# Optimization experiments

Measured on AMD Instinct MI355X. Metric: run time of the kernel, lower is better.

## Reference

```python
import jax, jax.numpy as jnp
import numpy as np
import math

B, N, L, ED, H = 2, 32, 4, 64, 4   # graphs, nodes/graph, layers, embed_dim, heads
HD = ED // H
EPS = 1e-5


def _ln(x, g, b):
    m = x.mean(-1, keepdims=True)
    v = ((x - m) ** 2).mean(-1, keepdims=True)
    return (x - m) * jax.lax.rsqrt(v + EPS) * g + b


def _layer(x, W, b, lg, lb, fW, fb, fg, fbeta):
    # NOTE: in the torch source, ModuleList([Linear]*4) shares ONE linear for
    # q/k/v1/v2 and ONE LayerNorm for norms[0..2]; we reproduce that sharing.
    h = (x @ W.T + b).reshape(B, N, N, H, HD)
    q = _ln(h, lg, lb)                                    # q == k (shared LN)
    scores = jnp.einsum('bxahd,bayhd->bxayh', q, q) / math.sqrt(HD)
    att = jax.nn.softmax(scores, axis=2)                  # softmax over 'a'
    xu = jnp.einsum('bxahd,bayhd->bxayhd', h, h)          # v1 == v2 == h
    xu = _ln(xu, lg, lb)                                  # shared LN again
    xu = jnp.einsum('bxayh,bxayhd->bxyhd', att, xu).reshape(B, N, N, ED)
    y = jnp.concatenate([x, xu], axis=-1) @ fW.T + fb
    return _ln(y, fg, fbeta)


def _diag_offdiag_maxpool(x):
    # x: (B, ED, N, N)
    diag = jnp.diagonal(x, axis1=-2, axis2=-1)            # (B, ED, N)
    max_diag = diag.max(axis=2)                           # (B, ED)
    val = jnp.abs(max_diag.max() + (-x).max())
    eye = jnp.eye(N, dtype=x.dtype)
    max_offdiag = (x - val * eye).max(axis=(2, 3))        # (B, ED)
    return jnp.concatenate([max_diag, max_offdiag], axis=1)  # (B, 2*ED)


def setup_inputs() -> dict:
    key = jax.random.key(0)
    ks = jax.random.split(key, 12)
    E = 1024
    g = jax.random.randint(ks[0], (E,), 0, B)
    ls = jax.random.randint(ks[1], (E,), 0, N)
    ld = jax.random.randint(ks[2], (E,), 0, N)
    edge_index = jnp.stack([g * N + ls, g * N + ld]).astype(jnp.int64)
    batch = (jnp.arange(B * N) // N).astype(jnp.int64)
    std = 0.02
    return {
        'edge_index': edge_index,
        'batch': batch,
        'W0': jax.random.normal(ks[3], (ED, 1), jnp.float32) * std,
        'b0': jnp.zeros((ED,), jnp.float32),
        'Ws': jax.random.normal(ks[4], (L - 1, ED, ED), jnp.float32) * std,
        'bs': jnp.zeros((L - 1, ED), jnp.float32),
        'ln_g': jnp.ones((L, HD), jnp.float32),
        'ln_b': jnp.zeros((L, HD), jnp.float32),
        'fW0': jax.random.normal(ks[5], (ED, 1 + ED), jnp.float32) * std,
        'fb0': jnp.zeros((ED,), jnp.float32),
        'fWs': jax.random.normal(ks[6], (L - 1, ED, 2 * ED), jnp.float32) * std,
        'fbs': jnp.zeros((L - 1, ED), jnp.float32),
        'fln_g': jnp.ones((L, ED), jnp.float32),
        'fln_b': jnp.zeros((L, ED), jnp.float32),
        'opW': jax.random.normal(ks[7], (L, ED // 2, 2 * ED), jnp.float32) * std,
        'opb': jnp.zeros((L, ED // 2), jnp.float32),
    }


def reference(edge_index, batch, W0, b0, Ws, bs, ln_g, ln_b,
              fW0, fb0, fWs, fbs, fln_g, fln_b, opW, opb):
    # to_dense_adj with edge_attr = 1.0
    g = batch[edge_index[0]]
    ls = edge_index[0] - g * N
    ld = edge_index[1] - g * N
    adj = jnp.zeros((B, N, N), jnp.float32).at[g, ls, ld].add(1.0)
    idx = jnp.arange(N)
    adj = adj.at[:, idx, idx].set(2.0)
    x = adj[..., None]                                    # (B, N, N, 1)

    scores = jnp.zeros((B, ED // 2), jnp.float32)
    for i in range(L):
        W = W0 if i == 0 else Ws[i - 1]
        b = b0 if i == 0 else bs[i - 1]
        fW = fW0 if i == 0 else fWs[i - 1]
        fb = fb0 if i == 0 else fbs[i - 1]
        x = _layer(x, W, b, ln_g[i], ln_b[i], fW, fb, fln_g[i], fln_b[i])
        pooled = _diag_offdiag_maxpool(jnp.transpose(x, (0, 3, 1, 2)))
        scores = scores + pooled @ opW[i].T + opb[i]

    # BatchNorm1d(momentum=1.0, affine=False), training mode -> batch stats
    m = scores.mean(axis=0)
    v = scores.var(axis=0)
    return (scores - m) / jnp.sqrt(v + EPS)
```

## Files before the change

### kernel.cpp

```cpp
#include <hip/hip_runtime.h>
#include <math.h>

#define EPS 1e-5f

#define AG_LOAD(p)     __hip_atomic_load((p), __ATOMIC_RELAXED, __HIP_MEMORY_SCOPE_AGENT)

__device__ __forceinline__ unsigned fenc(float f) {
    unsigned u = __float_as_uint(f);
    return (u & 0x80000000u) ? ~u : (u | 0x80000000u);
}
__device__ __forceinline__ float fdec(unsigned u) {
    u = (u & 0x80000000u) ? (u & 0x7FFFFFFFu) : ~u;
    return __uint_as_float(u);
}

struct Params {
    const int* ei; const int* batch; int E;
    const float* W0; const float* b0; const float* Ws; const float* bs;
    const float* ln_g; const float* ln_b;
    const float* fW0; const float* fb0; const float* fWs; const float* fbs;
    const float* fln_g; const float* fln_b;
    const float* opW; const float* opb;
    float* hA; float* hAT;
    float* hB; float* hBT;
    float* xbuf;
    unsigned* PdgU; unsigned* PoffU; unsigned* PmnU;
    int* bar;
    float* out;
};


__device__ __forceinline__ void pool_atomic(Params& p, int layer, int b_blk, int e,
                                            float mn, float off, float dg) {
    int o = layer * 128 + b_blk * 64 + e;
    atomicMax(&p.PdgU[o],  fenc(dg));
    atomicMax(&p.PoffU[o], fenc(off));
    atomicMax(&p.PmnU[o],  fenc(-mn));
}

__launch_bounds__(256, 2)
__global__ void k0(Params p) {
    const int tid  = threadIdx.x;
    const int blk  = blockIdx.x;
    const int gtid = blk * 256 + tid;
    const int c    = tid & 63;
    const int d    = c & 15;
    const int rl   = tid >> 6;
    const int rx   = rl >> 1;
    const int ry   = rl & 1;
    const int b_blk = blk >> 8;
    const int x0    = ((blk >> 4) & 15) * 2;
    const int y0    = (blk & 15) * 2;
    const int a_l  = c & 31;
    const int h1   = c >> 5;

    __shared__ float xslab2[2 * 32];
    __shared__ float yslab2[32 * 2];
    __shared__ __align__(16) float cA[64], cC[64], cW[64], cB0[64], cG[64], cBl[64];
    __shared__ float hstat[3][4];
    __shared__ float A1_s[4 * 132];
    __shared__ float K0h_s[4][4];
    __shared__ __align__(16) float xrow[4][64];
    __shared__ __align__(16) float xu_s[4][64];
    __shared__ float Wf0[64];
    __shared__ __align__(16) float T65[64 * 68];
    __shared__ __align__(16) float ST[64 * 68];

    if (tid < 64)  xslab2[tid] = 0.0f;
    if (tid >= 64 && tid < 128) yslab2[tid - 64] = 0.0f;

    if (tid < 64) {
        float Wc = p.W0[c], bc = p.b0[c];
        float sW = Wc, sB = bc;
        #pragma unroll
        for (int m = 1; m < 16; m <<= 1) {
            sW += __shfl_xor(sW, m, 16);
            sB += __shfl_xor(sB, m, 16);
        }
        float Ac = Wc - sW * 0.0625f;
        float Bc = bc - sB * 0.0625f;
        float sAA = Ac * Ac, sAB = Ac * Bc, sBB = Bc * Bc;
        #pragma unroll
        for (int m = 1; m < 16; m <<= 1) {
            sAA += __shfl_xor(sAA, m, 16);
            sAB += __shfl_xor(sAB, m, 16);
            sBB += __shfl_xor(sBB, m, 16);
        }
        cA[c] = Ac; cC[c] = Bc; cW[c] = Wc; cB0[c] = bc;
        cG[c] = p.ln_g[d]; cBl[c] = p.ln_b[d];
        if (d == 0) {
            hstat[0][c >> 4] = sAA * 0.0625f;
            hstat[1][c >> 4] = sAB * 0.0625f;
            hstat[2][c >> 4] = sBB * 0.0625f;
        }
        Wf0[tid] = p.fW0[tid * 65];
    }
    #pragma unroll
    for (int s = 0; s < 4; ++s) {
        int i = tid + s * 256;
        int cc = i >> 4, u = i & 15;
        const float* src = p.fW0 + cc * 65 + 1 + 4 * u;
        float4 w = make_float4(src[0], src[1], src[2], src[3]);
        *(float4*)(T65 + cc * 68 + 4 * ((u + 2 * cc) & 15)) = w;
    }
    #pragma unroll
    for (int s = 0; s < 4; ++s) {
        int i = tid + s * 256;
        float4 w = ((const float4*)p.Ws)[i];
        int cc = i >> 4, u = i & 15;
        *(float4*)(ST + cc * 68 + 4 * ((u + 2 * cc) & 15)) = w;
    }
    __syncthreads();

    for (int e2 = tid; e2 < p.E; e2 += 256) {
        int e0 = p.ei[e2], e1 = p.ei[p.E + e2];
        int g  = p.batch[e0];
        if (g == b_blk) {
            int ls = e0 - g * 32, ld = e1 - g * 32;
            unsigned dx = (unsigned)(ls - x0);
            if (dx < 2u) atomicAdd(&xslab2[dx * 32 + ld], 1.0f);
            unsigned dy = (unsigned)(ld - y0);
            if (dy < 2u) atomicAdd(&yslab2[ls * 2 + dy], 1.0f);
        }
    }
    __syncthreads();
    if (tid < 2)  xslab2[tid * 32 + x0 + tid] = 2.0f;
    if (tid >= 2 && tid < 4) { int j = tid - 2; yslab2[(y0 + j) * 2 + j] = 2.0f; }
    __syncthreads();

    const float vx = xslab2[rx * 32 + a_l];
    const float vy = yslab2[a_l * 2 + ry];
    float s0, s1, is0, is1, w0m, w1m;
    #pragma unroll
    for (int hb = 0; hb < 2; ++hb) {
        const int hh = h1 + 2 * hb;
        float rsx = rsqrtf(fmaf(fmaf(hstat[0][hh], vx, 2.0f * hstat[1][hh]), vx, hstat[2][hh]) + EPS);
        float rsy = rsqrtf(fmaf(fmaf(hstat[0][hh], vy, 2.0f * hstat[1][hh]), vy, hstat[2][hh]) + EPS);
        float qq = 0.f, sp = 0.f, sq = 0.f;
        #pragma unroll
        for (int t = 0; t < 4; ++t) {
            int dd = hh * 16 + 4 * t;
            float4 av = *(const float4*)(cA + dd);
            float4 bv = *(const float4*)(cC + dd);
            float4 wv = *(const float4*)(cW + dd);
            float4 b0v = *(const float4*)(cB0 + dd);
            float4 gv = *(const float4*)(cG + dd);
            float4 blv = *(const float4*)(cBl + dd);
            float qx, qy, pp;
            qx = fmaf(av.x, vx, bv.x) * rsx * gv.x + blv.x;
            qy = fmaf(av.x, vy, bv.x) * rsy * gv.x + blv.x;
            qq = fmaf(qx, qy, qq);
            pp = fmaf(wv.x, vx, b0v.x) * fmaf(wv.x, vy, b0v.x); sp += pp; sq += pp * pp;
            qx = fmaf(av.y, vx, bv.y) * rsx * gv.y + blv.y;
            qy = fmaf(av.y, vy, bv.y) * rsy * gv.y + blv.y;
            qq = fmaf(qx, qy, qq);
            pp = fmaf(wv.y, vx, b0v.y) * fmaf(wv.y, vy, b0v.y); sp += pp; sq += pp * pp;
            qx = fmaf(av.z, vx, bv.z) * rsx * gv.z + blv.z;
            qy = fmaf(av.z, vy, bv.z) * rsy * gv.z + blv.z;
            qq = fmaf(qx, qy, qq);
            pp = fmaf(wv.z, vx, b0v.z) * fmaf(wv.z, vy, b0v.z); sp += pp; sq += pp * pp;
            qx = fmaf(av.w, vx, bv.w) * rsx * gv.w + blv.w;
            qy = fmaf(av.w, vy, bv.w) * rsy * gv.w + blv.w;
            qq = fmaf(qx, qy, qq);
            pp = fmaf(wv.w, vx, b0v.w) * fmaf(wv.w, vy, b0v.w); sp += pp; sq += pp * pp;
        }
        float ss = qq * 0.25f;
        float mu = sp * 0.0625f, var = fmaxf(sq * 0.0625f - mu * mu, 0.f);
        float is = rsqrtf(var + EPS);
        if (hb == 0) { s0 = ss; is0 = is; w0m = mu * is; }
        else         { s1 = ss; is1 = is; w1m = mu * is; }
    }

    float m0 = s0, m1 = s1;
    #pragma unroll
    for (int m = 1; m < 32; m <<= 1) {
        m0 = fmaxf(m0, __shfl_xor(m0, m));
        m1 = fmaxf(m1, __shfl_xor(m1, m));
    }
    float e0 = __expf(s0 - m0), e1 = __expf(s1 - m1);
    float l0 = e0, l1 = e1, k0a = e0 * w0m, k1a = e1 * w1m;
    #pragma unroll
    for (int m = 1; m < 32; m <<= 1) {
        l0 += __shfl_xor(l0, m);  l1 += __shfl_xor(l1, m);
        k0a += __shfl_xor(k0a, m); k1a += __shfl_xor(k1a, m);
    }
    A1_s[rl * 132 + h1 * 33 + a_l]       = e0 * is0 / l0;
    A1_s[rl * 132 + (h1 + 2) * 33 + a_l] = e1 * is1 / l1;
    if (a_l == 0) {
        K0h_s[rl][h1]     = k0a / l0;
        K0h_s[rl][h1 + 2] = k1a / l1;
    }

    {
        const int hc = c >> 4;
        const float Wc = cW[c], bc = cB0[c];
        float acc = 0.f;
        #pragma unroll
        for (int a = 0; a < 32; ++a) {
            float vx2 = xslab2[rx * 32 + a];
            float vy2 = yslab2[a * 2 + ry];
            float pv = fmaf(Wc, vx2, bc) * fmaf(Wc, vy2, bc);
            acc = fmaf(A1_s[rl * 132 + hc * 33 + a], pv, acc);
        }
        xu_s[rl][c] = (acc - K0h_s[rl][hc]) * cG[c] + cBl[c];
    }

    const float adjv = xslab2[rx * 32 + y0 + ry];
    float acc2 = fmaf(Wf0[c], adjv, p.fb0[c]);
    #pragma unroll
    for (int u = 0; u < 16; ++u) {
        float4 w = *(const float4*)(T65 + c * 68 + 4 * ((u + 2 * c) & 15));
        float4 xr = *(const float4*)(&xu_s[rl][4 * u]);
        acc2 = fmaf(w.x, xr.x, acc2); acc2 = fmaf(w.y, xr.y, acc2);
        acc2 = fmaf(w.z, xr.z, acc2); acc2 = fmaf(w.w, xr.w, acc2);
    }
    float t1 = acc2;
    #pragma unroll
    for (int m = 1; m < 64; m <<= 1) t1 += __shfl_xor(t1, m, 64);
    float mu = t1 * (1.0f / 64.0f);
    float dv2 = acc2 - mu;
    float t2 = dv2 * dv2;
    #pragma unroll
    for (int m = 1; m < 64; m <<= 1) t2 += __shfl_xor(t2, m, 64);
    float xnew = dv2 * rsqrtf(t2 * (1.0f / 64.0f) + EPS) * p.fln_g[c] + p.fln_b[c];
    xrow[rl][c]  = xnew;
    p.xbuf[gtid] = xnew;
    __syncthreads();

    if (tid < 64) {
        float mn = 1e30f, off = -1e30f, dg = -1e30f;
        #pragma unroll
        for (int r2 = 0; r2 < 4; ++r2) {
            float v = xrow[r2][tid];
            mn = fminf(mn, v);
            if (x0 + (r2 >> 1) == y0 + (r2 & 1)) dg = fmaxf(dg, v);
            else off = fmaxf(off, v);
        }
        pool_atomic(p, 0, b_blk, tid, mn, off, dg);
    }

    {
        float acc = p.bs[c];
        #pragma unroll
        for (int u = 0; u < 16; ++u) {
            float4 w = *(const float4*)(ST + c * 68 + 4 * ((u + 2 * c) & 15));
            float4 xr = *(const float4*)(&xrow[rl][4 * u]);
            acc = fmaf(w.x, xr.x, acc); acc = fmaf(w.y, xr.y, acc);
            acc = fmaf(w.z, xr.z, acc); acc = fmaf(w.w, xr.w, acc);
        }
        int x = x0 + rx, y = y0 + ry;
        p.hA[(b_blk * 1024 + x * 32 + y) * 64 + c] = acc;
        p.hAT[((b_blk * 32 + y) * 32 + x) * 64 + c] = acc;
    }
}

__launch_bounds__(256, 2)
__global__ void klayer(Params p, int layer, int is_last) {
    const int tid  = threadIdx.x;
    const int blk  = blockIdx.x;
    const int gtid = blk * 256 + tid;
    const int c    = tid & 63;
    const int d    = c & 15;
    const int rl   = tid >> 6;
    const int rx   = rl >> 1;
    const int ry   = rl & 1;
    const int b_blk = blk >> 8;
    const int x0    = ((blk >> 4) & 15) * 2;
    const int y0    = (blk & 15) * 2;
    const int a_l  = c & 31;
    const int h1   = c >> 5;

    const float* hin  = (layer == 2) ? p.hB  : p.hA;
    const float* hinT = (layer == 2) ? p.hBT : p.hAT;
    float* hout  = (layer == 1) ? p.hB  : p.hA;
    float* houtT = (layer == 1) ? p.hBT : p.hAT;

    __shared__ __align__(16) float hx2_s[2][2176];
    __shared__ __align__(16) float yT2_s[2][2176];
    __shared__ __align__(16) float FT[64 * 132];
    __shared__ float A1_s[4 * 132];
    __shared__ float K0h_s[4][4];
    __shared__ __align__(16) float xrow[4][64];
    __shared__ __align__(16) float xu_s[4][64];
    __shared__ __align__(16) float g16[16], b16[16];
    __shared__ float vals[4];
    __shared__ float scores_s[64];
    __shared__ int tailflag;
    float* sm_mn  = &hx2_s[0][0];
    float* sm_off = sm_mn + 512;
    float* sm_dg  = sm_mn + 1024;
    float* psum   = sm_mn + 1536;

    float xv = p.xbuf[gtid];
    {
        const float4* sx0 = (const float4*)(hin + (b_blk * 1024 + x0 * 32) * 64);
        const float4* sx1 = (const float4*)(hin + (b_blk * 1024 + (x0 + 1) * 32) * 64);
        const float4* sy0 = (const float4*)(hinT + (b_blk * 32 + y0) * 2048);
        const float4* sy1 = (const float4*)(hinT + (b_blk * 32 + y0 + 1) * 2048);
        #pragma unroll
        for (int s = 0; s < 2; ++s) {
            int ii = tid + s * 256;
            int a = ii >> 4, u = ii & 15, pr = (u + 2 * a) & 15;
            *(float4*)(&hx2_s[0][a * 68 + 4 * pr]) = sx0[ii];
            *(float4*)(&hx2_s[1][a * 68 + 4 * pr]) = sx1[ii];
            *(float4*)(&yT2_s[0][a * 68 + 4 * pr]) = sy0[ii];
            *(float4*)(&yT2_s[1][a * 68 + 4 * pr]) = sy1[ii];
        }
    }
    if (tid < 16) {
        g16[tid] = p.ln_g[layer * 16 + tid];
        b16[tid] = p.ln_b[layer * 16 + tid];
    }
    {
        const float4* fw = (const float4*)(p.fWs + (layer - 1) * 8192);
        #pragma unroll
        for (int s = 0; s < 8; ++s) {
            int i = tid + s * 256;
            float4 w = fw[i];
            int cc = i >> 5, u = i & 31;
            *(float4*)(FT + cc * 132 + 4 * ((u + 2 * cc) & 31)) = w;
        }
    }
    xrow[rl][c] = xv;
    __syncthreads();

    float s0, s1, is0, is1, w0m, w1m;
    #pragma unroll
    for (int hb = 0; hb < 2; ++hb) {
        const int hh = h1 + 2 * hb;
        float4 xh4[4], yh4[4];
        float sxp = 0.f, sxq = 0.f, syp = 0.f, syq = 0.f;
        #pragma unroll
        for (int t = 0; t < 4; ++t) {
            int ps = 4 * (((hh * 4 + t) + 2 * a_l) & 15);
            float4 v = *(const float4*)(&hx2_s[rx][a_l * 68 + ps]);
            float4 y = *(const float4*)(&yT2_s[ry][a_l * 68 + ps]);
            xh4[t] = v; yh4[t] = y;
            sxp += v.x + v.y + v.z + v.w;
            sxq += v.x*v.x + v.y*v.y + v.z*v.z + v.w*v.w;
            syp += y.x + y.y + y.z + y.w;
            syq += y.x*y.x + y.y*y.y + y.z*y.z + y.w*y.w;
        }
        float mxm = sxp * 0.0625f;
        float rsx = rsqrtf(fmaxf(sxq * 0.0625f - mxm * mxm, 0.f) + EPS);
        float mym = syp * 0.0625f;
        float rsy = rsqrtf(fmaxf(syq * 0.0625f - mym * mym, 0.f) + EPS);
        float qq = 0.f, sp = 0.f, sq = 0.f;
        #pragma unroll
        for (int t = 0; t < 4; ++t) {
            float4 g4 = *(const float4*)(g16 + 4 * t);
            float4 b4 = *(const float4*)(b16 + 4 * t);
            float4 xh = xh4[t], yh = yh4[t];
            float qx, qy, pp;
            qx = (xh.x - mxm) * rsx * g4.x + b4.x;
            qy = (yh.x - mym) * rsy * g4.x + b4.x;
            qq = fmaf(qx, qy, qq);  pp = xh.x * yh.x; sp += pp; sq += pp * pp;
            qx = (xh.y - mxm) * rsx * g4.y + b4.y;
            qy = (yh.y - mym) * rsy * g4.y + b4.y;
            qq = fmaf(qx, qy, qq);  pp = xh.y * yh.y; sp += pp; sq += pp * pp;
            qx = (xh.z - mxm) * rsx * g4.z + b4.z;
            qy = (yh.z - mym) * rsy * g4.z + b4.z;
            qq = fmaf(qx, qy, qq);  pp = xh.z * yh.z; sp += pp; sq += pp * pp;
            qx = (xh.w - mxm) * rsx * g4.w + b4.w;
            qy = (yh.w - mym) * rsy * g4.w + b4.w;
            qq = fmaf(qx, qy, qq);  pp = xh.w * yh.w; sp += pp; sq += pp * pp;
        }
        float ss = qq * 0.25f;
        float mu = sp * 0.0625f, var = fmaxf(sq * 0.0625f - mu * mu, 0.f);
        float is = rsqrtf(var + EPS);
        if (hb == 0) { s0 = ss; is0 = is; w0m = mu * is; }
        else         { s1 = ss; is1 = is; w1m = mu * is; }
    }

    float m0 = s0, m1 = s1;
    #pragma unroll
    for (int m = 1; m < 32; m <<= 1) {
        m0 = fmaxf(m0, __shfl_xor(m0, m));
        m1 = fmaxf(m1, __shfl_xor(m1, m));
    }
    float e0 = __expf(s0 - m0), e1 = __expf(s1 - m1);
    float l0 = e0, l1 = e1, k0a = e0 * w0m, k1a = e1 * w1m;
    #pragma unroll
    for (int m = 1; m < 32; m <<= 1) {
        l0 += __shfl_xor(l0, m);  l1 += __shfl_xor(l1, m);
        k0a += __shfl_xor(k0a, m); k1a += __shfl_xor(k1a, m);
    }
    A1_s[rl * 132 + h1 * 33 + a_l]       = e0 * is0 / l0;
    A1_s[rl * 132 + (h1 + 2) * 33 + a_l] = e1 * is1 / l1;
    if (a_l == 0) {
        K0h_s[rl][h1]     = k0a / l0;
        K0h_s[rl][h1 + 2] = k1a / l1;
    }

    {
        const int hc = c >> 4;
        const int ce = c & 3;
        float acc = 0.f;
        #pragma unroll
        for (int a = 0; a < 32; ++a) {
            int ps = 4 * (((c >> 2) + 2 * a) & 15) + ce;
            float hxv = hx2_s[rx][a * 68 + ps];
            float hyv = yT2_s[ry][a * 68 + ps];
            acc = fmaf(A1_s[rl * 132 + hc * 33 + a], hxv * hyv, acc);
        }
        xu_s[rl][c] = (acc - K0h_s[rl][hc]) * g16[d] + b16[d];
    }

    float acc2 = p.fbs[(layer - 1) * 64 + c];
    #pragma unroll
    for (int u = 0; u < 16; ++u) {
        float4 w = *(const float4*)(FT + c * 132 + 4 * ((u + 2 * c) & 31));
        float4 xr = *(const float4*)(&xrow[rl][4 * u]);
        acc2 = fmaf(w.x, xr.x, acc2); acc2 = fmaf(w.y, xr.y, acc2);
        acc2 = fmaf(w.z, xr.z, acc2); acc2 = fmaf(w.w, xr.w, acc2);
    }
    #pragma unroll
    for (int u = 16; u < 32; ++u) {
        float4 w = *(const float4*)(FT + c * 132 + 4 * ((u + 2 * c) & 31));
        float4 xr = *(const float4*)(&xu_s[rl][4 * (u - 16)]);
        acc2 = fmaf(w.x, xr.x, acc2); acc2 = fmaf(w.y, xr.y, acc2);
        acc2 = fmaf(w.z, xr.z, acc2); acc2 = fmaf(w.w, xr.w, acc2);
    }
    float t1 = acc2;
    #pragma unroll
    for (int m = 1; m < 64; m <<= 1) t1 += __shfl_xor(t1, m, 64);
    float mu = t1 * (1.0f / 64.0f);
    float dv2 = acc2 - mu;
    float t2 = dv2 * dv2;
    #pragma unroll
    for (int m = 1; m < 64; m <<= 1) t2 += __shfl_xor(t2, m, 64);
    float xnew = dv2 * rsqrtf(t2 * (1.0f / 64.0f) + EPS) *
                 p.fln_g[layer * 64 + c] + p.fln_b[layer * 64 + c];
    __syncthreads();
    xrow[rl][c] = xnew;
    if (!is_last) {
        p.xbuf[gtid] = xnew;
        const float4* sw = (const float4*)(p.Ws + layer * 4096);
        #pragma unroll
        for (int s = 0; s < 4; ++s) {
            int i = tid + s * 256;
            float4 w = sw[i];
            int cc = i >> 4, u = i & 15;
            *(float4*)(FT + cc * 68 + 4 * ((u + 2 * cc) & 15)) = w;
        }
    }
    __syncthreads();

    if (tid < 64) {
        float mn = 1e30f, off = -1e30f, dg = -1e30f;
        #pragma unroll
        for (int r2 = 0; r2 < 4; ++r2) {
            float v = xrow[r2][tid];
            mn = fminf(mn, v);
            if (x0 + (r2 >> 1) == y0 + (r2 & 1)) dg = fmaxf(dg, v);
            else off = fmaxf(off, v);
        }
        pool_atomic(p, layer, b_blk, tid, mn, off, dg);
    }

    if (!is_last) {
        float acc = p.bs[layer * 64 + c];
        #pragma unroll
        for (int u = 0; u < 16; ++u) {
            float4 w = *(const float4*)(FT + c * 68 + 4 * ((u + 2 * c) & 15));
            float4 xr = *(const float4*)(&xrow[rl][4 * u]);
            acc = fmaf(w.x, xr.x, acc); acc = fmaf(w.y, xr.y, acc);
            acc = fmaf(w.z, xr.z, acc); acc = fmaf(w.w, xr.w, acc);
        }
        int x = x0 + rx, y = y0 + ry;
        hout[(b_blk * 1024 + x * 32 + y) * 64 + c] = acc;
        houtT[((b_blk * 32 + y) * 32 + x) * 64 + c] = acc;
        return;
    }

    __syncthreads();
    if (tid == 0) {
        int r = __hip_atomic_fetch_add(p.bar, 1, __ATOMIC_RELAXED,
                                       __HIP_MEMORY_SCOPE_AGENT);
        tailflag = (r == 511) ? 1 : 0;
    }
    __syncthreads();
    if (!tailflag) return;

    #pragma unroll
    for (int s = 0; s < 2; ++s) {
        int slot = tid + s * 256;
        unsigned ud = AG_LOAD(&p.PdgU[slot]);
        unsigned uo = AG_LOAD(&p.PoffU[slot]);
        unsigned um = AG_LOAD(&p.PmnU[slot]);
        sm_dg[slot]  = fdec(ud);
        sm_off[slot] = fdec(uo);
        sm_mn[slot]  = -fdec(um);
    }
    __syncthreads();
    if (tid < 4) {
        float gmx = -1e30f, gmn = 1e30f;
        for (int i2 = 0; i2 < 128; ++i2) {
            gmx = fmaxf(gmx, sm_dg[tid * 128 + i2]);
            gmn = fminf(gmn, sm_mn[tid * 128 + i2]);
        }
        vals[tid] = fabsf(gmx - gmn);
    }
    __syncthreads();
    {
        int bb = tid >> 7, cc = (tid >> 2) & 31, pp = tid & 3;
        float a2 = 0.0f;
        for (int l = 0; l < 4; ++l) {
            float val = vals[l];
            const float* Wr = p.opW + l * 4096 + cc * 128;
            int base = l * 128 + bb * 64;
            for (int j = pp * 32; j < pp * 32 + 32; ++j) {
                float pv;
                if (j < 64) pv = sm_dg[base + j];
                else        pv = fmaxf(sm_off[base + j - 64], sm_dg[base + j - 64] - val);
                a2 = fmaf(Wr[j], pv, a2);
            }
        }
        psum[tid] = a2;
    }
    __syncthreads();
    if (tid < 64) {
        int bb = tid >> 5, cc = tid & 31;
        float a2 = 0.0f;
        for (int l = 0; l < 4; ++l) a2 += p.opb[l * 32 + cc];
        for (int pp = 0; pp < 4; ++pp) a2 += psum[bb * 128 + cc * 4 + pp];
        scores_s[tid] = a2;
    }
    __syncthreads();
    if (tid < 32) {
        float sA = scores_s[tid], sB = scores_s[32 + tid];
        float mu2 = 0.5f * (sA + sB);
        float va = 0.5f * ((sA - mu2) * (sA - mu2) + (sB - mu2) * (sB - mu2));
        float inv = rsqrtf(va + EPS);
        p.out[tid]      = (sA - mu2) * inv;
        p.out[32 + tid] = (sB - mu2) * inv;
    }
}

extern "C" void kernel_launch(void* const* d_in, const int* in_sizes, int n_in,
                              void* d_out, int out_size, void* d_ws, size_t ws_size,
                              hipStream_t stream) {
    Params prm;
    prm.ei    = (const int*)d_in[0];
    prm.batch = (const int*)d_in[1];
    prm.E     = in_sizes[0] / 2;
    prm.W0    = (const float*)d_in[2];
    prm.b0    = (const float*)d_in[3];
    prm.Ws    = (const float*)d_in[4];
    prm.bs    = (const float*)d_in[5];
    prm.ln_g  = (const float*)d_in[6];
    prm.ln_b  = (const float*)d_in[7];
    prm.fW0   = (const float*)d_in[8];
    prm.fb0   = (const float*)d_in[9];
    prm.fWs   = (const float*)d_in[10];
    prm.fbs   = (const float*)d_in[11];
    prm.fln_g = (const float*)d_in[12];
    prm.fln_b = (const float*)d_in[13];
    prm.opW   = (const float*)d_in[14];
    prm.opb   = (const float*)d_in[15];

    float* ws = (float*)d_ws;
    prm.hA    = ws;
    prm.hAT   = prm.hA   + 131072;
    prm.hB    = prm.hAT  + 131072;
    prm.hBT   = prm.hB   + 131072;
    prm.xbuf  = prm.hBT  + 131072;
    unsigned* pu = (unsigned*)(prm.xbuf + 131072);
    prm.PdgU  = pu;
    prm.PoffU = pu + 512;
    prm.PmnU  = pu + 1024;
    prm.bar   = (int*)(pu + 1536);
    prm.out   = (float*)d_out;

    hipMemsetAsync(pu, 0, 1552 * sizeof(unsigned), stream);
    k0<<<512, 256, 0, stream>>>(prm);
    klayer<<<512, 256, 0, stream>>>(prm, 1, 0);
    klayer<<<512, 256, 0, stream>>>(prm, 2, 0);
    klayer<<<512, 256, 0, stream>>>(prm, 3, 1);
}
```

Baseline: 160.7 us.

## Fuse all layer kernels into one persistent kernel with hierarchical grid barriers

```diff
diff --git a/kernel.cpp b/kernel.cpp
--- a/kernel.cpp
+++ b/kernel.cpp
@@ -4,6 +4,7 @@
 #define EPS 1e-5f
 
 #define AG_LOAD(p)     __hip_atomic_load((p), __ATOMIC_RELAXED, __HIP_MEMORY_SCOPE_AGENT)
+#define AG_STORE(p, v) __hip_atomic_store((p), (v), __ATOMIC_RELAXED, __HIP_MEMORY_SCOPE_AGENT)
 
 __device__ __forceinline__ unsigned fenc(float f) {
     unsigned u = __float_as_uint(f);
@@ -12,6 +13,18 @@
 __device__ __forceinline__ float fdec(unsigned u) {
     u = (u & 0x80000000u) ? (u & 0x7FFFFFFFu) : ~u;
     return __uint_as_float(u);
+}
+
+__device__ __forceinline__ float4 ag_load4(const float* ptr) {
+    const unsigned long long* q = (const unsigned long long*)ptr;
+    unsigned long long lo = AG_LOAD(q);
+    unsigned long long hi = AG_LOAD(q + 1);
+    float4 w;
+    w.x = __uint_as_float((unsigned)lo);
+    w.y = __uint_as_float((unsigned)(lo >> 32));
+    w.z = __uint_as_float((unsigned)hi);
+    w.w = __uint_as_float((unsigned)(hi >> 32));
+    return w;
 }
 
 struct Params {
@@ -23,12 +36,25 @@
     const float* opW; const float* opb;
     float* hA; float* hAT;
     float* hB; float* hBT;
-    float* xbuf;
     unsigned* PdgU; unsigned* PoffU; unsigned* PmnU;
     int* bar;
     float* out;
 };
 
+__device__ __forceinline__ void gridbar(int* bar, int ph, int blk) {
+    __syncthreads();
+    if (threadIdx.x == 0) {
+        int* base = bar + ph * 160;
+        int g = blk >> 6;
+        int r = atomicAdd(base + g * 16, 1);
+        if (r == 63) {
+            int r2 = atomicAdd(base + 128, 1);
+            if (r2 == 7) AG_STORE(base + 144, 1);
+        }
+        while (AG_LOAD(base + 144) == 0) __builtin_amdgcn_s_sleep(8);
+    }
+    __syncthreads();
+}
 
 __device__ __forceinline__ void pool_atomic(Params& p, int layer, int b_blk, int e,
                                             float mn, float off, float dg) {
@@ -39,10 +65,9 @@
 }
 
 __launch_bounds__(256, 2)
-__global__ void k0(Params p) {
+__global__ void kfused(Params p) {
     const int tid  = threadIdx.x;
     const int blk  = blockIdx.x;
-    const int gtid = blk * 256 + tid;
     const int c    = tid & 63;
     const int d    = c & 15;
     const int rl   = tid >> 6;
@@ -58,13 +83,21 @@
     __shared__ float yslab2[32 * 2];
     __shared__ __align__(16) float cA[64], cC[64], cW[64], cB0[64], cG[64], cBl[64];
     __shared__ float hstat[3][4];
+    __shared__ float Wf0[64];
+    __shared__ __align__(16) float hx2_s[2][2176];
+    __shared__ __align__(16) float yT2_s[2][2176];
+    __shared__ __align__(16) float WB[8704];
     __shared__ float A1_s[4 * 132];
     __shared__ float K0h_s[4][4];
     __shared__ __align__(16) float xrow[4][64];
     __shared__ __align__(16) float xu_s[4][64];
-    __shared__ float Wf0[64];
-    __shared__ __align__(16) float T65[64 * 68];
-    __shared__ __align__(16) float ST[64 * 68];
+    __shared__ __align__(16) float g16[16], b16[16];
+    __shared__ float vals[4];
+    __shared__ float scores_s[64];
+    float* sm_mn  = &hx2_s[0][0];
+    float* sm_off = sm_mn + 512;
+    float* sm_dg  = sm_mn + 1024;
+    float* psum   = sm_mn + 1536;
 
     if (tid < 64)  xslab2[tid] = 0.0f;
     if (tid >= 64 && tid < 128) yslab2[tid - 64] = 0.0f;
@@ -101,14 +134,14 @@
         int cc = i >> 4, u = i & 15;
         const float* src = p.fW0 + cc * 65 + 1 + 4 * u;
         float4 w = make_float4(src[0], src[1], src[2], src[3]);
-        *(float4*)(T65 + cc * 68 + 4 * ((u + 2 * cc) & 15)) = w;
+        *(float4*)(WB + cc * 68 + 4 * ((u + 2 * cc) & 15)) = w;
     }
     #pragma unroll
     for (int s = 0; s < 4; ++s) {
         int i = tid + s * 256;
         float4 w = ((const float4*)p.Ws)[i];
         int cc = i >> 4, u = i & 15;
-        *(float4*)(ST + cc * 68 + 4 * ((u + 2 * cc) & 15)) = w;
+        *(float4*)(WB + 4352 + cc * 68 + 4 * ((u + 2 * cc) & 15)) = w;
     }
     __syncthreads();
 
@@ -128,103 +161,104 @@
     if (tid >= 2 && tid < 4) { int j = tid - 2; yslab2[(y0 + j) * 2 + j] = 2.0f; }
     __syncthreads();
 
-    const float vx = xslab2[rx * 32 + a_l];
-    const float vy = yslab2[a_l * 2 + ry];
-    float s0, s1, is0, is1, w0m, w1m;
-    #pragma unroll
-    for (int hb = 0; hb < 2; ++hb) {
-        const int hh = h1 + 2 * hb;
-        float rsx = rsqrtf(fmaf(fmaf(hstat[0][hh], vx, 2.0f * hstat[1][hh]), vx, hstat[2][hh]) + EPS);
-        float rsy = rsqrtf(fmaf(fmaf(hstat[0][hh], vy, 2.0f * hstat[1][hh]), vy, hstat[2][hh]) + EPS);
-        float qq = 0.f, sp = 0.f, sq = 0.f;
-        #pragma unroll
-        for (int t = 0; t < 4; ++t) {
-            int dd = hh * 16 + 4 * t;
-            float4 av = *(const float4*)(cA + dd);
-            float4 bv = *(const float4*)(cC + dd);
-            float4 wv = *(const float4*)(cW + dd);
-            float4 b0v = *(const float4*)(cB0 + dd);
-            float4 gv = *(const float4*)(cG + dd);
-            float4 blv = *(const float4*)(cBl + dd);
-            float qx, qy, pp;
-            qx = fmaf(av.x, vx, bv.x) * rsx * gv.x + blv.x;
-            qy = fmaf(av.x, vy, bv.x) * rsy * gv.x + blv.x;
-            qq = fmaf(qx, qy, qq);
-            pp = fmaf(wv.x, vx, b0v.x) * fmaf(wv.x, vy, b0v.x); sp += pp; sq += pp * pp;
-            qx = fmaf(av.y, vx, bv.y) * rsx * gv.y + blv.y;
-            qy = fmaf(av.y, vy, bv.y) * rsy * gv.y + blv.y;
-            qq = fmaf(qx, qy, qq);
-            pp = fmaf(wv.y, vx, b0v.y) * fmaf(wv.y, vy, b0v.y); sp += pp; sq += pp * pp;
-            qx = fmaf(av.z, vx, bv.z) * rsx * gv.z + blv.z;
-            qy = fmaf(av.z, vy, bv.z) * rsy * gv.z + blv.z;
-            qq = fmaf(qx, qy, qq);
-            pp = fmaf(wv.z, vx, b0v.z) * fmaf(wv.z, vy, b0v.z); sp += pp; sq += pp * pp;
-            qx = fmaf(av.w, vx, bv.w) * rsx * gv.w + blv.w;
-            qy = fmaf(av.w, vy, bv.w) * rsy * gv.w + blv.w;
-            qq = fmaf(qx, qy, qq);
-            pp = fmaf(wv.w, vx, b0v.w) * fmaf(wv.w, vy, b0v.w); sp += pp; sq += pp * pp;
-        }
-        float ss = qq * 0.25f;
-        float mu = sp * 0.0625f, var = fmaxf(sq * 0.0625f - mu * mu, 0.f);
-        float is = rsqrtf(var + EPS);
-        if (hb == 0) { s0 = ss; is0 = is; w0m = mu * is; }
-        else         { s1 = ss; is1 = is; w1m = mu * is; }
-    }
-
-    float m0 = s0, m1 = s1;
-    #pragma unroll
-    for (int m = 1; m < 32; m <<= 1) {
-        m0 = fmaxf(m0, __shfl_xor(m0, m));
-        m1 = fmaxf(m1, __shfl_xor(m1, m));
-    }
-    float e0 = __expf(s0 - m0), e1 = __expf(s1 - m1);
-    float l0 = e0, l1 = e1, k0a = e0 * w0m, k1a = e1 * w1m;
-    #pragma unroll
-    for (int m = 1; m < 32; m <<= 1) {
-        l0 += __shfl_xor(l0, m);  l1 += __shfl_xor(l1, m);
-        k0a += __shfl_xor(k0a, m); k1a += __shfl_xor(k1a, m);
-    }
-    A1_s[rl * 132 + h1 * 33 + a_l]       = e0 * is0 / l0;
-    A1_s[rl * 132 + (h1 + 2) * 33 + a_l] = e1 * is1 / l1;
-    if (a_l == 0) {
-        K0h_s[rl][h1]     = k0a / l0;
-        K0h_s[rl][h1 + 2] = k1a / l1;
-    }
-
     {
-        const int hc = c >> 4;
-        const float Wc = cW[c], bc = cB0[c];
-        float acc = 0.f;
-        #pragma unroll
-        for (int a = 0; a < 32; ++a) {
-            float vx2 = xslab2[rx * 32 + a];
-            float vy2 = yslab2[a * 2 + ry];
-            float pv = fmaf(Wc, vx2, bc) * fmaf(Wc, vy2, bc);
-            acc = fmaf(A1_s[rl * 132 + hc * 33 + a], pv, acc);
-        }
-        xu_s[rl][c] = (acc - K0h_s[rl][hc]) * cG[c] + cBl[c];
-    }
-
-    const float adjv = xslab2[rx * 32 + y0 + ry];
-    float acc2 = fmaf(Wf0[c], adjv, p.fb0[c]);
-    #pragma unroll
-    for (int u = 0; u < 16; ++u) {
-        float4 w = *(const float4*)(T65 + c * 68 + 4 * ((u + 2 * c) & 15));
-        float4 xr = *(const float4*)(&xu_s[rl][4 * u]);
-        acc2 = fmaf(w.x, xr.x, acc2); acc2 = fmaf(w.y, xr.y, acc2);
-        acc2 = fmaf(w.z, xr.z, acc2); acc2 = fmaf(w.w, xr.w, acc2);
-    }
-    float t1 = acc2;
-    #pragma unroll
-    for (int m = 1; m < 64; m <<= 1) t1 += __shfl_xor(t1, m, 64);
-    float mu = t1 * (1.0f / 64.0f);
-    float dv2 = acc2 - mu;
-    float t2 = dv2 * dv2;
-    #pragma unroll
-    for (int m = 1; m < 64; m <<= 1) t2 += __shfl_xor(t2, m, 64);
-    float xnew = dv2 * rsqrtf(t2 * (1.0f / 64.0f) + EPS) * p.fln_g[c] + p.fln_b[c];
-    xrow[rl][c]  = xnew;
-    p.xbuf[gtid] = xnew;
+        const float vx = xslab2[rx * 32 + a_l];
+        const float vy = yslab2[a_l * 2 + ry];
+        float s0, s1, is0, is1, w0m, w1m;
+        #pragma unroll
+        for (int hb = 0; hb < 2; ++hb) {
+            const int hh = h1 + 2 * hb;
+            float rsx = rsqrtf(fmaf(fmaf(hstat[0][hh], vx, 2.0f * hstat[1][hh]), vx, hstat[2][hh]) + EPS);
+            float rsy = rsqrtf(fmaf(fmaf(hstat[0][hh], vy, 2.0f * hstat[1][hh]), vy, hstat[2][hh]) + EPS);
+            float qq = 0.f, sp = 0.f, sq = 0.f;
+            #pragma unroll
+            for (int t = 0; t < 4; ++t) {
+                int dd = hh * 16 + 4 * t;
+                float4 av = *(const float4*)(cA + dd);
+                float4 bv = *(const float4*)(cC + dd);
+                float4 wv = *(const float4*)(cW + dd);
+                float4 b0v = *(const float4*)(cB0 + dd);
+                float4 gv = *(const float4*)(cG + dd);
+                float4 blv = *(const float4*)(cBl + dd);
+                float qx, qy, pp;
+                qx = fmaf(av.x, vx, bv.x) * rsx * gv.x + blv.x;
+                qy = fmaf(av.x, vy, bv.x) * rsy * gv.x + blv.x;
+                qq = fmaf(qx, qy, qq);
+                pp = fmaf(wv.x, vx, b0v.x) * fmaf(wv.x, vy, b0v.x); sp += pp; sq += pp * pp;
+                qx = fmaf(av.y, vx, bv.y) * rsx * gv.y + blv.y;
+                qy = fmaf(av.y, vy, bv.y) * rsy * gv.y + blv.y;
+                qq = fmaf(qx, qy, qq);
+                pp = fmaf(wv.y, vx, b0v.y) * fmaf(wv.y, vy, b0v.y); sp += pp; sq += pp * pp;
+                qx = fmaf(av.z, vx, bv.z) * rsx * gv.z + blv.z;
+                qy = fmaf(av.z, vy, bv.z) * rsy * gv.z + blv.z;
+                qq = fmaf(qx, qy, qq);
+                pp = fmaf(wv.z, vx, b0v.z) * fmaf(wv.z, vy, b0v.z); sp += pp; sq += pp * pp;
+                qx = fmaf(av.w, vx, bv.w) * rsx * gv.w + blv.w;
+                qy = fmaf(av.w, vy, bv.w) * rsy * gv.w + blv.w;
+                qq = fmaf(qx, qy, qq);
+                pp = fmaf(wv.w, vx, b0v.w) * fmaf(wv.w, vy, b0v.w); sp += pp; sq += pp * pp;
+            }
+            float ss = qq * 0.25f;
+            float mu = sp * 0.0625f, var = fmaxf(sq * 0.0625f - mu * mu, 0.f);
+            float is = rsqrtf(var + EPS);
+            if (hb == 0) { s0 = ss; is0 = is; w0m = mu * is; }
+            else         { s1 = ss; is1 = is; w1m = mu * is; }
+        }
+
+        float m0 = s0, m1 = s1;
+        #pragma unroll
+        for (int m = 1; m < 32; m <<= 1) {
+            m0 = fmaxf(m0, __shfl_xor(m0, m));
+            m1 = fmaxf(m1, __shfl_xor(m1, m));
+        }
+        float e0 = __expf(s0 - m0), e1 = __expf(s1 - m1);
+        float l0 = e0, l1 = e1, k0a = e0 * w0m, k1a = e1 * w1m;
+        #pragma unroll
+        for (int m = 1; m < 32; m <<= 1) {
+            l0 += __shfl_xor(l0, m);  l1 += __shfl_xor(l1, m);
+            k0a += __shfl_xor(k0a, m); k1a += __shfl_xor(k1a, m);
+        }
+        A1_s[rl * 132 + h1 * 33 + a_l]       = e0 * is0 / l0;
+        A1_s[rl * 132 + (h1 + 2) * 33 + a_l] = e1 * is1 / l1;
+        if (a_l == 0) {
+            K0h_s[rl][h1]     = k0a / l0;
+            K0h_s[rl][h1 + 2] = k1a / l1;
+        }
+
+        {
+            const int hc = c >> 4;
+            const float Wc = cW[c], bc = cB0[c];
+            float acc = 0.f;
+            #pragma unroll
+            for (int a = 0; a < 32; ++a) {
+                float vx2 = xslab2[rx * 32 + a];
+                float vy2 = yslab2[a * 2 + ry];
+                float pv = fmaf(Wc, vx2, bc) * fmaf(Wc, vy2, bc);
+                acc = fmaf(A1_s[rl * 132 + hc * 33 + a], pv, acc);
+            }
+            xu_s[rl][c] = (acc - K0h_s[rl][hc]) * cG[c] + cBl[c];
+        }
+
+        const float adjv = xslab2[rx * 32 + y0 + ry];
+        float acc2 = fmaf(Wf0[c], adjv, p.fb0[c]);
+        #pragma unroll
+        for (int u = 0; u < 16; ++u) {
+            float4 w = *(const float4*)(WB + c * 68 + 4 * ((u + 2 * c) & 15));
+            float4 xr = *(const float4*)(&xu_s[rl][4 * u]);
+            acc2 = fmaf(w.x, xr.x, acc2); acc2 = fmaf(w.y, xr.y, acc2);
+            acc2 = fmaf(w.z, xr.z, acc2); acc2 = fmaf(w.w, xr.w, acc2);
+        }
+        float t1 = acc2;
+        #pragma unroll
+        for (int m = 1; m < 64; m <<= 1) t1 += __shfl_xor(t1, m, 64);
+        float mu = t1 * (1.0f / 64.0f);
+        float dv2 = acc2 - mu;
+        float t2 = dv2 * dv2;
+        #pragma unroll
+        for (int m = 1; m < 64; m <<= 1) t2 += __shfl_xor(t2, m, 64);
+        float xnew = dv2 * rsqrtf(t2 * (1.0f / 64.0f) + EPS) * p.fln_g[c] + p.fln_b[c];
+        xrow[rl][c] = xnew;
+    }
     __syncthreads();
 
     if (tid < 64) {
@@ -238,249 +272,209 @@
         }
         pool_atomic(p, 0, b_blk, tid, mn, off, dg);
     }
-
     {
         float acc = p.bs[c];
         #pragma unroll
         for (int u = 0; u < 16; ++u) {
-            float4 w = *(const float4*)(ST + c * 68 + 4 * ((u + 2 * c) & 15));
+            float4 w = *(const float4*)(WB + 4352 + c * 68 + 4 * ((u + 2 * c) & 15));
             float4 xr = *(const float4*)(&xrow[rl][4 * u]);
             acc = fmaf(w.x, xr.x, acc); acc = fmaf(w.y, xr.y, acc);
             acc = fmaf(w.z, xr.z, acc); acc = fmaf(w.w, xr.w, acc);
         }
         int x = x0 + rx, y = y0 + ry;
-        p.hA[(b_blk * 1024 + x * 32 + y) * 64 + c] = acc;
-        p.hAT[((b_blk * 32 + y) * 32 + x) * 64 + c] = acc;
-    }
-}
-
-__launch_bounds__(256, 2)
-__global__ void klayer(Params p, int layer, int is_last) {
-    const int tid  = threadIdx.x;
-    const int blk  = blockIdx.x;
-    const int gtid = blk * 256 + tid;
-    const int c    = tid & 63;
-    const int d    = c & 15;
-    const int rl   = tid >> 6;
-    const int rx   = rl >> 1;
-    const int ry   = rl & 1;
-    const int b_blk = blk >> 8;
-    const int x0    = ((blk >> 4) & 15) * 2;
-    const int y0    = (blk & 15) * 2;
-    const int a_l  = c & 31;
-    const int h1   = c >> 5;
-
-    const float* hin  = (layer == 2) ? p.hB  : p.hA;
-    const float* hinT = (layer == 2) ? p.hBT : p.hAT;
-    float* hout  = (layer == 1) ? p.hB  : p.hA;
-    float* houtT = (layer == 1) ? p.hBT : p.hAT;
-
-    __shared__ __align__(16) float hx2_s[2][2176];
-    __shared__ __align__(16) float yT2_s[2][2176];
-    __shared__ __align__(16) float FT[64 * 132];
-    __shared__ float A1_s[4 * 132];
-    __shared__ float K0h_s[4][4];
-    __shared__ __align__(16) float xrow[4][64];
-    __shared__ __align__(16) float xu_s[4][64];
-    __shared__ __align__(16) float g16[16], b16[16];
-    __shared__ float vals[4];
-    __shared__ float scores_s[64];
-    __shared__ int tailflag;
-    float* sm_mn  = &hx2_s[0][0];
-    float* sm_off = sm_mn + 512;
-    float* sm_dg  = sm_mn + 1024;
-    float* psum   = sm_mn + 1536;
-
-    float xv = p.xbuf[gtid];
-    {
-        const float4* sx0 = (const float4*)(hin + (b_blk * 1024 + x0 * 32) * 64);
-        const float4* sx1 = (const float4*)(hin + (b_blk * 1024 + (x0 + 1) * 32) * 64);
-        const float4* sy0 = (const float4*)(hinT + (b_blk * 32 + y0) * 2048);
-        const float4* sy1 = (const float4*)(hinT + (b_blk * 32 + y0 + 1) * 2048);
-        #pragma unroll
-        for (int s = 0; s < 2; ++s) {
-            int ii = tid + s * 256;
-            int a = ii >> 4, u = ii & 15, pr = (u + 2 * a) & 15;
-            *(float4*)(&hx2_s[0][a * 68 + 4 * pr]) = sx0[ii];
-            *(float4*)(&hx2_s[1][a * 68 + 4 * pr]) = sx1[ii];
-            *(float4*)(&yT2_s[0][a * 68 + 4 * pr]) = sy0[ii];
-            *(float4*)(&yT2_s[1][a * 68 + 4 * pr]) = sy1[ii];
-        }
-    }
-    if (tid < 16) {
-        g16[tid] = p.ln_g[layer * 16 + tid];
-        b16[tid] = p.ln_b[layer * 16 + tid];
-    }
-    {
-        const float4* fw = (const float4*)(p.fWs + (layer - 1) * 8192);
-        #pragma unroll
-        for (int s = 0; s < 8; ++s) {
-            int i = tid + s * 256;
-            float4 w = fw[i];
-            int cc = i >> 5, u = i & 31;
-            *(float4*)(FT + cc * 132 + 4 * ((u + 2 * cc) & 31)) = w;
-        }
-    }
-    xrow[rl][c] = xv;
-    __syncthreads();
-
-    float s0, s1, is0, is1, w0m, w1m;
-    #pragma unroll
-    for (int hb = 0; hb < 2; ++hb) {
-        const int hh = h1 + 2 * hb;
-        float4 xh4[4], yh4[4];
-        float sxp = 0.f, sxq = 0.f, syp = 0.f, syq = 0.f;
-        #pragma unroll
-        for (int t = 0; t < 4; ++t) {
-            int ps = 4 * (((hh * 4 + t) + 2 * a_l) & 15);
-            float4 v = *(const float4*)(&hx2_s[rx][a_l * 68 + ps]);
-            float4 y = *(const float4*)(&yT2_s[ry][a_l * 68 + ps]);
-            xh4[t] = v; yh4[t] = y;
-            sxp += v.x + v.y + v.z + v.w;
-            sxq += v.x*v.x + v.y*v.y + v.z*v.z + v.w*v.w;
-            syp += y.x + y.y + y.z + y.w;
-            syq += y.x*y.x + y.y*y.y + y.z*y.z + y.w*y.w;
-        }
-        float mxm = sxp * 0.0625f;
-        float rsx = rsqrtf(fmaxf(sxq * 0.0625f - mxm * mxm, 0.f) + EPS);
-        float mym = syp * 0.0625f;
-        float rsy = rsqrtf(fmaxf(syq * 0.0625f - mym * mym, 0.f) + EPS);
-        float qq = 0.f, sp = 0.f, sq = 0.f;
-        #pragma unroll
-        for (int t = 0; t < 4; ++t) {
-            float4 g4 = *(const float4*)(g16 + 4 * t);
-            float4 b4 = *(const float4*)(b16 + 4 * t);
-            float4 xh = xh4[t], yh = yh4[t];
-            float qx, qy, pp;
-            qx = (xh.x - mxm) * rsx * g4.x + b4.x;
-            qy = (yh.x - mym) * rsy * g4.x + b4.x;
-            qq = fmaf(qx, qy, qq);  pp = xh.x * yh.x; sp += pp; sq += pp * pp;
-            qx = (xh.y - mxm) * rsx * g4.y + b4.y;
-            qy = (yh.y - mym) * rsy * g4.y + b4.y;
-            qq = fmaf(qx, qy, qq);  pp = xh.y * yh.y; sp += pp; sq += pp * pp;
-            qx = (xh.z - mxm) * rsx * g4.z + b4.z;
-            qy = (yh.z - mym) * rsy * g4.z + b4.z;
-            qq = fmaf(qx, qy, qq);  pp = xh.z * yh.z; sp += pp; sq += pp * pp;
-            qx = (xh.w - mxm) * rsx * g4.w + b4.w;
-            qy = (yh.w - mym) * rsy * g4.w + b4.w;
-            qq = fmaf(qx, qy, qq);  pp = xh.w * yh.w; sp += pp; sq += pp * pp;
-        }
-        float ss = qq * 0.25f;
-        float mu = sp * 0.0625f, var = fmaxf(sq * 0.0625f - mu * mu, 0.f);
-        float is = rsqrtf(var + EPS);
-        if (hb == 0) { s0 = ss; is0 = is; w0m = mu * is; }
-        else         { s1 = ss; is1 = is; w1m = mu * is; }
-    }
-
-    float m0 = s0, m1 = s1;
-    #pragma unroll
-    for (int m = 1; m < 32; m <<= 1) {
-        m0 = fmaxf(m0, __shfl_xor(m0, m));
-        m1 = fmaxf(m1, __shfl_xor(m1, m));
-    }
-    float e0 = __expf(s0 - m0), e1 = __expf(s1 - m1);
-    float l0 = e0, l1 = e1, k0a = e0 * w0m, k1a = e1 * w1m;
-    #pragma unroll
-    for (int m = 1; m < 32; m <<= 1) {
-        l0 += __shfl_xor(l0, m);  l1 += __shfl_xor(l1, m);
-        k0a += __shfl_xor(k0a, m); k1a += __shfl_xor(k1a, m);
-    }
-    A1_s[rl * 132 + h1 * 33 + a_l]       = e0 * is0 / l0;
-    A1_s[rl * 132 + (h1 + 2) * 33 + a_l] = e1 * is1 / l1;
-    if (a_l == 0) {
-        K0h_s[rl][h1]     = k0a / l0;
-        K0h_s[rl][h1 + 2] = k1a / l1;
-    }
-
-    {
-        const int hc = c >> 4;
-        const int ce = c & 3;
-        float acc = 0.f;
-        #pragma unroll
-        for (int a = 0; a < 32; ++a) {
-            int ps = 4 * (((c >> 2) + 2 * a) & 15) + ce;
-            float hxv = hx2_s[rx][a * 68 + ps];
-            float hyv = yT2_s[ry][a * 68 + ps];
-            acc = fmaf(A1_s[rl * 132 + hc * 33 + a], hxv * hyv, acc);
-        }
-        xu_s[rl][c] = (acc - K0h_s[rl][hc]) * g16[d] + b16[d];
-    }
-
-    float acc2 = p.fbs[(layer - 1) * 64 + c];
-    #pragma unroll
-    for (int u = 0; u < 16; ++u) {
-        float4 w = *(const float4*)(FT + c * 132 + 4 * ((u + 2 * c) & 31));
-        float4 xr = *(const float4*)(&xrow[rl][4 * u]);
-        acc2 = fmaf(w.x, xr.x, acc2); acc2 = fmaf(w.y, xr.y, acc2);
-        acc2 = fmaf(w.z, xr.z, acc2); acc2 = fmaf(w.w, xr.w, acc2);
-    }
-    #pragma unroll
-    for (int u = 16; u < 32; ++u) {
-        float4 w = *(const float4*)(FT + c * 132 + 4 * ((u + 2 * c) & 31));
-        float4 xr = *(const float4*)(&xu_s[rl][4 * (u - 16)]);
-        acc2 = fmaf(w.x, xr.x, acc2); acc2 = fmaf(w.y, xr.y, acc2);
-        acc2 = fmaf(w.z, xr.z, acc2); acc2 = fmaf(w.w, xr.w, acc2);
-    }
-    float t1 = acc2;
-    #pragma unroll
-    for (int m = 1; m < 64; m <<= 1) t1 += __shfl_xor(t1, m, 64);
-    float mu = t1 * (1.0f / 64.0f);
-    float dv2 = acc2 - mu;
-    float t2 = dv2 * dv2;
-    #pragma unroll
-    for (int m = 1; m < 64; m <<= 1) t2 += __shfl_xor(t2, m, 64);
-    float xnew = dv2 * rsqrtf(t2 * (1.0f / 64.0f) + EPS) *
-                 p.fln_g[layer * 64 + c] + p.fln_b[layer * 64 + c];
-    __syncthreads();
-    xrow[rl][c] = xnew;
-    if (!is_last) {
-        p.xbuf[gtid] = xnew;
-        const float4* sw = (const float4*)(p.Ws + layer * 4096);
-        #pragma unroll
-        for (int s = 0; s < 4; ++s) {
-            int i = tid + s * 256;
-            float4 w = sw[i];
-            int cc = i >> 4, u = i & 15;
-            *(float4*)(FT + cc * 68 + 4 * ((u + 2 * cc) & 15)) = w;
-        }
-    }
-    __syncthreads();
-
-    if (tid < 64) {
-        float mn = 1e30f, off = -1e30f, dg = -1e30f;
-        #pragma unroll
-        for (int r2 = 0; r2 < 4; ++r2) {
-            float v = xrow[r2][tid];
-            mn = fminf(mn, v);
-            if (x0 + (r2 >> 1) == y0 + (r2 & 1)) dg = fmaxf(dg, v);
-            else off = fmaxf(off, v);
-        }
-        pool_atomic(p, layer, b_blk, tid, mn, off, dg);
-    }
-
-    if (!is_last) {
-        float acc = p.bs[layer * 64 + c];
+        AG_STORE(&p.hA[(b_blk * 1024 + x * 32 + y) * 64 + c], acc);
+        AG_STORE(&p.hAT[((b_blk * 32 + y) * 32 + x) * 64 + c], acc);
+    }
+    gridbar(p.bar, 0, blk);
+
+    #pragma unroll 1
+    for (int layer = 1; layer <= 3; ++layer) {
+        const float* hin  = (layer == 2) ? p.hB  : p.hA;
+        const float* hinT = (layer == 2) ? p.hBT : p.hAT;
+        float* hout  = (layer == 1) ? p.hB  : p.hA;
+        float* houtT = (layer == 1) ? p.hBT : p.hAT;
+
+        {
+            const float* sx0 = hin + (b_blk * 1024 + x0 * 32) * 64;
+            const float* sx1 = hin + (b_blk * 1024 + (x0 + 1) * 32) * 64;
+            const float* sy0 = hinT + (b_blk * 32 + y0) * 2048;
+            const float* sy1 = hinT + (b_blk * 32 + y0 + 1) * 2048;
+            #pragma unroll
+            for (int s = 0; s < 2; ++s) {
+                int ii = tid + s * 256;
+                int a = ii >> 4, u = ii & 15, pr = (u + 2 * a) & 15;
+                *(float4*)(&hx2_s[0][a * 68 + 4 * pr]) = ag_load4(sx0 + ii * 4);
+                *(float4*)(&hx2_s[1][a * 68 + 4 * pr]) = ag_load4(sx1 + ii * 4);
+                *(float4*)(&yT2_s[0][a * 68 + 4 * pr]) = ag_load4(sy0 + ii * 4);
+                *(float4*)(&yT2_s[1][a * 68 + 4 * pr]) = ag_load4(sy1 + ii * 4);
+            }
+        }
+        if (tid < 16) {
+            g16[tid] = p.ln_g[layer * 16 + tid];
+            b16[tid] = p.ln_b[layer * 16 + tid];
+        }
+        {
+            const float4* fw = (const float4*)(p.fWs + (layer - 1) * 8192);
+            #pragma unroll
+            for (int s = 0; s < 8; ++s) {
+                int i = tid + s * 256;
+                float4 w = fw[i];
+                int cc = i >> 5, u = i & 31;
+                *(float4*)(WB + cc * 132 + 4 * ((u + 2 * cc) & 31)) = w;
+            }
+        }
+        __syncthreads();
+
+        float s0, s1, is0, is1, w0m, w1m;
+        #pragma unroll
+        for (int hb = 0; hb < 2; ++hb) {
+            const int hh = h1 + 2 * hb;
+            float4 xh4[4], yh4[4];
+            float sxp = 0.f, sxq = 0.f, syp = 0.f, syq = 0.f;
+            #pragma unroll
+            for (int t = 0; t < 4; ++t) {
+                int ps = 4 * (((hh * 4 + t) + 2 * a_l) & 15);
+                float4 v = *(const float4*)(&hx2_s[rx][a_l * 68 + ps]);
+                float4 y = *(const float4*)(&yT2_s[ry][a_l * 68 + ps]);
+                xh4[t] = v; yh4[t] = y;
+                sxp += v.x + v.y + v.z + v.w;
+                sxq += v.x*v.x + v.y*v.y + v.z*v.z + v.w*v.w;
+                syp += y.x + y.y + y.z + y.w;
+                syq += y.x*y.x + y.y*y.y + y.z*y.z + y.w*y.w;
+            }
+            float mxm = sxp * 0.0625f;
+            float rsx = rsqrtf(fmaxf(sxq * 0.0625f - mxm * mxm, 0.f) + EPS);
+            float mym = syp * 0.0625f;
+            float rsy = rsqrtf(fmaxf(syq * 0.0625f - mym * mym, 0.f) + EPS);
+            float qq = 0.f, sp = 0.f, sq = 0.f;
+            #pragma unroll
+            for (int t = 0; t < 4; ++t) {
+                float4 g4 = *(const float4*)(g16 + 4 * t);
+                float4 b4 = *(const float4*)(b16 + 4 * t);
+                float4 xh = xh4[t], yh = yh4[t];
+                float qx, qy, pp;
+                qx = (xh.x - mxm) * rsx * g4.x + b4.x;
+                qy = (yh.x - mym) * rsy * g4.x + b4.x;
+                qq = fmaf(qx, qy, qq);  pp = xh.x * yh.x; sp += pp; sq += pp * pp;
+                qx = (xh.y - mxm) * rsx * g4.y + b4.y;
+                qy = (yh.y - mym) * rsy * g4.y + b4.y;
+                qq = fmaf(qx, qy, qq);  pp = xh.y * yh.y; sp += pp; sq += pp * pp;
+                qx = (xh.z - mxm) * rsx * g4.z + b4.z;
+                qy = (yh.z - mym) * rsy * g4.z + b4.z;
+                qq = fmaf(qx, qy, qq);  pp = xh.z * yh.z; sp += pp; sq += pp * pp;
+                qx = (xh.w - mxm) * rsx * g4.w + b4.w;
+                qy = (yh.w - mym) * rsy * g4.w + b4.w;
+                qq = fmaf(qx, qy, qq);  pp = xh.w * yh.w; sp += pp; sq += pp * pp;
+            }
+            float ss = qq * 0.25f;
+            float mu = sp * 0.0625f, var = fmaxf(sq * 0.0625f - mu * mu, 0.f);
+            float is = rsqrtf(var + EPS);
+            if (hb == 0) { s0 = ss; is0 = is; w0m = mu * is; }
+            else         { s1 = ss; is1 = is; w1m = mu * is; }
+        }
+
+        float m0 = s0, m1 = s1;
+        #pragma unroll
+        for (int m = 1; m < 32; m <<= 1) {
+            m0 = fmaxf(m0, __shfl_xor(m0, m));
+            m1 = fmaxf(m1, __shfl_xor(m1, m));
+        }
+        float e0 = __expf(s0 - m0), e1 = __expf(s1 - m1);
+        float l0 = e0, l1 = e1, k0a = e0 * w0m, k1a = e1 * w1m;
+        #pragma unroll
+        for (int m = 1; m < 32; m <<= 1) {
+            l0 += __shfl_xor(l0, m);  l1 += __shfl_xor(l1, m);
+            k0a += __shfl_xor(k0a, m); k1a += __shfl_xor(k1a, m);
+        }
+        A1_s[rl * 132 + h1 * 33 + a_l]       = e0 * is0 / l0;
+        A1_s[rl * 132 + (h1 + 2) * 33 + a_l] = e1 * is1 / l1;
+        if (a_l == 0) {
+            K0h_s[rl][h1]     = k0a / l0;
+            K0h_s[rl][h1 + 2] = k1a / l1;
+        }
+
+        {
+            const int hc = c >> 4;
+            const int ce = c & 3;
+            float acc = 0.f;
+            #pragma unroll
+            for (int a = 0; a < 32; ++a) {
+                int ps = 4 * (((c >> 2) + 2 * a) & 15) + ce;
+                float hxv = hx2_s[rx][a * 68 + ps];
+                float hyv = yT2_s[ry][a * 68 + ps];
+                acc = fmaf(A1_s[rl * 132 + hc * 33 + a], hxv * hyv, acc);
+            }
+            xu_s[rl][c] = (acc - K0h_s[rl][hc]) * g16[d] + b16[d];
+        }
+
+        float acc2 = p.fbs[(layer - 1) * 64 + c];
         #pragma unroll
         for (int u = 0; u < 16; ++u) {
-            float4 w = *(const float4*)(FT + c * 68 + 4 * ((u + 2 * c) & 15));
+            float4 w = *(const float4*)(WB + c * 132 + 4 * ((u + 2 * c) & 31));
             float4 xr = *(const float4*)(&xrow[rl][4 * u]);
-            acc = fmaf(w.x, xr.x, acc); acc = fmaf(w.y, xr.y, acc);
-            acc = fmaf(w.z, xr.z, acc); acc = fmaf(w.w, xr.w, acc);
-        }
-        int x = x0 + rx, y = y0 + ry;
-        hout[(b_blk * 1024 + x * 32 + y) * 64 + c] = acc;
-        houtT[((b_blk * 32 + y) * 32 + x) * 64 + c] = acc;
-        return;
-    }
-
-    __syncthreads();
-    if (tid == 0) {
-        int r = __hip_atomic_fetch_add(p.bar, 1, __ATOMIC_RELAXED,
-                                       __HIP_MEMORY_SCOPE_AGENT);
-        tailflag = (r == 511) ? 1 : 0;
-    }
-    __syncthreads();
-    if (!tailflag) return;
+            acc2 = fmaf(w.x, xr.x, acc2); acc2 = fmaf(w.y, xr.y, acc2);
+            acc2 = fmaf(w.z, xr.z, acc2); acc2 = fmaf(w.w, xr.w, acc2);
+        }
+        #pragma unroll
+        for (int u = 16; u < 32; ++u) {
+            float4 w = *(const float4*)(WB + c * 132 + 4 * ((u + 2 * c) & 31));
+            float4 xr = *(const float4*)(&xu_s[rl][4 * (u - 16)]);
+            acc2 = fmaf(w.x, xr.x, acc2); acc2 = fmaf(w.y, xr.y, acc2);
+            acc2 = fmaf(w.z, xr.z, acc2); acc2 = fmaf(w.w, xr.w, acc2);
+        }
+        float t1 = acc2;
+        #pragma unroll
+        for (int m = 1; m < 64; m <<= 1) t1 += __shfl_xor(t1, m, 64);
+        float mu = t1 * (1.0f / 64.0f);
+        float dv2 = acc2 - mu;
+        float t2 = dv2 * dv2;
+        #pragma unroll
+        for (int m = 1; m < 64; m <<= 1) t2 += __shfl_xor(t2, m, 64);
+        float xnew = dv2 * rsqrtf(t2 * (1.0f / 64.0f) + EPS) *
+                     p.fln_g[layer * 64 + c] + p.fln_b[layer * 64 + c];
+        __syncthreads();
+        xrow[rl][c] = xnew;
+        if (layer < 3) {
+            const float4* sw = (const float4*)(p.Ws + layer * 4096);
+            #pragma unroll
+            for (int s = 0; s < 4; ++s) {
+                int i = tid + s * 256;
+                float4 w = sw[i];
+                int cc = i >> 4, u = i & 15;
+                *(float4*)(WB + cc * 68 + 4 * ((u + 2 * cc) & 15)) = w;
+            }
+        }
+        __syncthreads();
+
+        if (tid < 64) {
+            float mn = 1e30f, off = -1e30f, dg = -1e30f;
+            #pragma unroll
+            for (int r2 = 0; r2 < 4; ++r2) {
+                float v = xrow[r2][tid];
+                mn = fminf(mn, v);
+                if (x0 + (r2 >> 1) == y0 + (r2 & 1)) dg = fmaxf(dg, v);
+                else off = fmaxf(off, v);
+            }
+            pool_atomic(p, layer, b_blk, tid, mn, off, dg);
+        }
+
+        if (layer < 3) {
+            float acc = p.bs[layer * 64 + c];
+            #pragma unroll
+            for (int u = 0; u < 16; ++u) {
+                float4 w = *(const float4*)(WB + c * 68 + 4 * ((u + 2 * c) & 15));
+                float4 xr = *(const float4*)(&xrow[rl][4 * u]);
+                acc = fmaf(w.x, xr.x, acc); acc = fmaf(w.y, xr.y, acc);
+                acc = fmaf(w.z, xr.z, acc); acc = fmaf(w.w, xr.w, acc);
+            }
+            int x = x0 + rx, y = y0 + ry;
+            AG_STORE(&hout[(b_blk * 1024 + x * 32 + y) * 64 + c], acc);
+            AG_STORE(&houtT[((b_blk * 32 + y) * 32 + x) * 64 + c], acc);
+        }
+        gridbar(p.bar, layer, blk);
+    }
+
+    if (blk != 0) return;
 
     #pragma unroll
     for (int s = 0; s < 2; ++s) {
@@ -561,20 +555,16 @@
 
     float* ws = (float*)d_ws;
     prm.hA    = ws;
-    prm.hAT   = prm.hA   + 131072;
-    prm.hB    = prm.hAT  + 131072;
-    prm.hBT   = prm.hB   + 131072;
-    prm.xbuf  = prm.hBT  + 131072;
-    unsigned* pu = (unsigned*)(prm.xbuf + 131072);
+    prm.hAT   = prm.hA  + 131072;
+    prm.hB    = prm.hAT + 131072;
+    prm.hBT   = prm.hB  + 131072;
+    unsigned* pu = (unsigned*)(prm.hBT + 131072);
     prm.PdgU  = pu;
     prm.PoffU = pu + 512;
     prm.PmnU  = pu + 1024;
     prm.bar   = (int*)(pu + 1536);
     prm.out   = (float*)d_out;
 
-    hipMemsetAsync(pu, 0, 1552 * sizeof(unsigned), stream);
-    k0<<<512, 256, 0, stream>>>(prm);
-    klayer<<<512, 256, 0, stream>>>(prm, 1, 0);
-    klayer<<<512, 256, 0, stream>>>(prm, 2, 0);
-    klayer<<<512, 256, 0, stream>>>(prm, 3, 1);
-}
+    hipMemsetAsync(pu, 0, (1536 + 640) * sizeof(unsigned), stream);
+    kfused<<<512, 256, 0, stream>>>(prm);
+}
```

Result: slower. 169.6 us (+5.5%).
